# Kernel optimization log

Measured on AMD Instinct MI355X. Metric: run time of the kernel, lower is better.

Reference implementation:

```python
import jax, jax.numpy as jnp
import numpy as np

B, S, DQK, DV, H = 4, 2048, 128, 128, 8


def setup_inputs() -> dict:
    key = jax.random.key(0)
    ks = jax.random.split(key, 9)
    s = 0.02
    return {
        "query": jax.random.normal(ks[0], (B, S, DQK), jnp.float32),
        "key": jax.random.normal(ks[1], (B, S, DQK), jnp.float32),
        "value": jax.random.normal(ks[2], (B, S, DV), jnp.float32),
        "WQ": jax.random.normal(ks[3], (DQK, H * DQK), jnp.float32) * s,
        "bQ": jax.random.normal(ks[4], (H * DQK,), jnp.float32) * s,
        "WK": jax.random.normal(ks[5], (DQK, H * DQK), jnp.float32) * s,
        "bK": jax.random.normal(ks[6], (H * DQK,), jnp.float32) * s,
        "WV": jax.random.normal(ks[7], (DV, H * DV), jnp.float32) * s,
        "bV": jax.random.normal(ks[8], (H * DV,), jnp.float32) * s,
    }


def reference(query, key, value, WQ, bQ, WK, bK, WV, bV):
    b, qn, dqk = query.shape
    kn = key.shape[1]
    dv = value.shape[2]
    h = H
    # projections -> [b, n, h, d]
    Q = (query @ WQ + bQ).reshape(b, qn, h, dqk)
    K = (key @ WK + bK).reshape(b, kn, h, dqk)
    V = (value @ WV + bV).reshape(b, kn, h, dv)
    # abs(QK^T)/sqrt(dk) score -- non-standard, prevents flash kernels
    scores = jnp.abs(jnp.einsum("bqhd,bkhd->bhqk", Q, K)) / jnp.sqrt(
        jnp.asarray(dqk, query.dtype)
    )
    w = jax.nn.softmax(scores, axis=-1)  # [b,h,q,k]
    # (complex cast +0j in the original is numerically a no-op on real V)
    out = jnp.einsum("bhqk,bkhd->bqhd", w, V).reshape(b, qn, h * dv)
    return out
```

## Files before the change

### kernel.cpp

```cpp
#include <hip/hip_runtime.h>
#include <hip/hip_bf16.h>

#define B_ 4
#define S_ 2048
#define D_ 128
#define H_ 8

typedef __attribute__((ext_vector_type(8))) short bf16x8;
typedef __attribute__((ext_vector_type(4))) float f32x4;

__device__ __forceinline__ short f2bf(float f) {
  union { float f; unsigned u; } v; v.f = f;
  unsigned u = v.u;
  unsigned r = (u + 0x7FFFu + ((u >> 16) & 1u)) >> 16;
  return (short)r;
}

__device__ __forceinline__ short4 pack4(f32x4 p) {
  union { __hip_bfloat162 h2[2]; short4 s4; } u;
  u.h2[0] = __float22bfloat162_rn(make_float2(p[0], p[1]));
  u.h2[1] = __float22bfloat162_rn(make_float2(p[2], p[3]));
  return u.s4;
}

__global__ __launch_bounds__(256) void prep(
    const float* __restrict__ WQ, const float* __restrict__ WK, const float* __restrict__ WV,
    short* __restrict__ FQ, short* __restrict__ FK, short* __restrict__ FV) {
  __shared__ float tile[64][65];
  int bw = blockIdx.x >> 5;
  int tl = blockIdx.x & 31;
  int n0 = (tl & 15) * 64, k0 = (tl >> 4) * 64;
  const float* W = (bw == 0) ? WQ : (bw == 1) ? WK : WV;
  short* WF = (bw == 0) ? FQ : (bw == 1) ? FK : FV;
#pragma unroll
  for (int i = 0; i < 16; ++i) {
    int cix = threadIdx.x + 256 * i;
    int rr = cix >> 6, cc = cix & 63;
    tile[rr][cc] = W[(k0 + rr) * 1024 + n0 + cc];
  }
  __syncthreads();
#pragma unroll
  for (int i = 0; i < 16; ++i) {
    int cix = threadIdx.x + 256 * i;
    int rr = cix >> 6, cc = cix & 63;
    int n = n0 + rr, k = k0 + cc;
    size_t off = (size_t)(n >> 7) * 16384
               + (size_t)(((n >> 4) & 7) * 4 + (k >> 5)) * 512
               + ((k >> 3) & 3) * 128 + (n & 15) * 8 + (k & 7);
    WF[off] = f2bf(tile[cc][rr]);
  }
}

template <int MODE>
__device__ __forceinline__ void proj_tile(const float* __restrict__ X,
                                          const short* __restrict__ WF,
                                          const float* __restrict__ bias,
                                          short* __restrict__ out,
                                          int mtile, int ntile,
                                          short* sA) {
  int tid = threadIdx.x;
  int lane = tid & 63, w = tid >> 6;
  int l15 = lane & 15, l4 = lane >> 4;
  int m0 = mtile * 128, n0 = ntile * 128;

#pragma unroll
  for (int j = 0; j < 8; ++j) {
    int f = w * 8 + j;
    const float* src = X + (size_t)(m0 + (f >> 2) * 16 + l15) * 128 + (f & 3) * 32 + l4 * 8;
    float4 v0 = *(const float4*)src;
    float4 v1 = *(const float4*)(src + 4);
    union { struct { short4 lo, hi; } s; bf16x8 v; } u;
    u.s.lo = pack4((f32x4){v0.x, v0.y, v0.z, v0.w});
    u.s.hi = pack4((f32x4){v1.x, v1.y, v1.z, v1.w});
    *(bf16x8*)(sA + f * 512 + lane * 8) = u.v;
  }

  int wr = w >> 1, wc = w & 1;

  const short* wfb = WF + (size_t)ntile * 16384 + wc * 8192 + lane * 8;
  bf16x8 b[16];
#pragma unroll
  for (int q = 0; q < 16; ++q)
    b[q] = *(const bf16x8*)(wfb + q * 512);

  __syncthreads();

  f32x4 acc[4][4];
#pragma unroll
  for (int mi = 0; mi < 4; ++mi)
#pragma unroll
    for (int ni = 0; ni < 4; ++ni) acc[mi][ni] = (f32x4){0.f, 0.f, 0.f, 0.f};

#pragma unroll
  for (int mi = 0; mi < 4; ++mi) {
    bf16x8 a[4];
#pragma unroll
    for (int st = 0; st < 4; ++st)
      a[st] = *(const bf16x8*)(sA + ((wr * 4 + mi) * 4 + st) * 512 + lane * 8);
#pragma unroll
    for (int ni = 0; ni < 4; ++ni) {
#pragma unroll
      for (int st = 0; st < 4; ++st) {
        if (MODE <= 1)
          acc[mi][ni] = __builtin_amdgcn_mfma_f32_16x16x32_bf16(b[ni * 4 + st], a[st], acc[mi][ni], 0, 0, 0);
        else
          acc[mi][ni] = __builtin_amdgcn_mfma_f32_16x16x32_bf16(a[st], b[ni * 4 + st], acc[mi][ni], 0, 0, 0);
      }
    }
  }

  if (MODE == 0) {
#pragma unroll
    for (int mi = 0; mi < 4; ++mi) {
      int sg = m0 + wr * 64 + mi * 16 + l15;
      int bb = sg >> 11, s = sg & 2047;
      short* orow = out + ((size_t)(bb * H_ + ntile) * S_ + s) * D_;
#pragma unroll
      for (int ni = 0; ni < 4; ++ni) {
        int d0 = wc * 64 + ni * 16 + l4 * 4;
        float4 bv = *(const float4*)(bias + n0 + d0);
        f32x4 t = acc[mi][ni];
        t[0] += bv.x; t[1] += bv.y; t[2] += bv.z; t[3] += bv.w;
        *(short4*)(orow + d0) = pack4(t);
      }
    }
  } else if (MODE == 1) {
#pragma unroll
    for (int mi = 0; mi < 4; ++mi) {
      int key = m0 + wr * 64 + mi * 16 + l15;
      int bb = key >> 11, k = key & 2047;
      size_t base = (size_t)(bb * H_ + ntile) * (S_ * D_) + (size_t)(k >> 6) * 8192
                  + ((k >> 4) & 3) * 4 * 512 + (k & 15) * 8;
#pragma unroll
      for (int ni = 0; ni < 4; ++ni) {
        int d0 = wc * 64 + ni * 16 + l4 * 4;
        float4 bv = *(const float4*)(bias + n0 + d0);
        f32x4 t = acc[mi][ni];
        t[0] += bv.x; t[1] += bv.y; t[2] += bv.z; t[3] += bv.w;
        size_t off = base + (size_t)(d0 >> 5) * 512 + ((d0 >> 3) & 3) * 128 + (d0 & 7);
        *(short4*)(out + off) = pack4(t);
      }
    }
  } else {
#pragma unroll
    for (int ni = 0; ni < 4; ++ni) {
      int d = wc * 64 + ni * 16 + l15;
      float bvs = bias[n0 + d];
#pragma unroll
      for (int mi = 0; mi < 4; ++mi) {
        int sg0 = m0 + wr * 64 + mi * 16 + l4 * 4;
        int bb = sg0 >> 11, s0 = sg0 & 2047;
        f32x4 t = acc[mi][ni];
        t[0] += bvs; t[1] += bvs; t[2] += bvs; t[3] += bvs;
        size_t off = (size_t)(bb * H_ + ntile) * (S_ * D_)
                   + (size_t)(s0 >> 6) * 8192
                   + (size_t)((d >> 4) * 2 + ((s0 >> 5) & 1)) * 512
                   + ((s0 >> 3) & 3) * 128 + (d & 15) * 8
                   + (s0 & 7);
        *(short4*)(out + off) = pack4(t);
      }
    }
  }
}

__global__ __launch_bounds__(256, 3) void proj3(
    const float* __restrict__ xq, const float* __restrict__ xk, const float* __restrict__ xv,
    const short* __restrict__ wtq, const short* __restrict__ wtk, const short* __restrict__ wtv,
    const float* __restrict__ bQ, const float* __restrict__ bK, const float* __restrict__ bV,
    short* __restrict__ Qp, short* __restrict__ Kf, short* __restrict__ Vf) {
  __shared__ short sA[16384];
  int work = (blockIdx.x & 7) * 192 + (blockIdx.x >> 3);
  int which = work >> 9;
  int t = work & 511;
  int mtile = t >> 3, ntile = t & 7;
  if (which == 0)      proj_tile<0>(xq, wtq, bQ, Qp, mtile, ntile, sA);
  else if (which == 1) proj_tile<1>(xk, wtk, bK, Kf, mtile, ntile, sA);
  else                 proj_tile<2>(xv, wtv, bV, Vf, mtile, ntile, sA);
}

#define PSTR 72

#define HSTEP(KC, KN, H, DOISS)                                                \
  {                                                                            \
    if (DOISS) {                                                               \
      _Pragma("unroll") for (int j = 0; j < 8; ++j)                            \
        KN[j] = *(const bf16x8*)(kfb + ((H) + 1) * 4096 + j * 512);            \
    }                                                                          \
    bf16x8 bv[8];                                                              \
    _Pragma("unroll") for (int j = 0; j < 8; ++j)                              \
      bv[j] = *(const bf16x8*)(vfb + ((H) >> 1) * 8192 + (j * 2 + ((H) & 1)) * 512); \
    __builtin_amdgcn_sched_barrier(0);                                         \
    f32x4 s0[2], s1[2];                                                        \
    __builtin_amdgcn_s_setprio(1);                                             \
    _Pragma("unroll") for (int m = 0; m < 2; ++m) {                            \
      s0[m] = (f32x4){0.f, 0.f, 0.f, 0.f};                                     \
      s1[m] = (f32x4){0.f, 0.f, 0.f, 0.f};                                     \
      _Pragma("unroll") for (int st = 0; st < 4; ++st) {                       \
        s0[m] = __builtin_amdgcn_mfma_f32_16x16x32_bf16(KC[m * 4 + st], aq[0][st], s0[m], 0, 0, 0); \
        s1[m] = __builtin_amdgcn_mfma_f32_16x16x32_bf16(KC[m * 4 + st], aq[1][st], s1[m], 0, 0, 0); \
      }                                                                        \
    }                                                                          \
    __builtin_amdgcn_s_setprio(0);                                             \
    bf16x8 ap0, ap1;                                                           \
    _Pragma("unroll") for (int m = 0; m < 2; ++m) {                            \
      _Pragma("unroll") for (int r = 0; r < 4; ++r) {                          \
        float p = __builtin_amdgcn_exp2f(fabsf(s0[m][r]) * SC2);               \
        ls0 += p;                                                              \
        s0[m][r] = p;                                                          \
      }                                                                        \
      *(short4*)(pw + l15 * PSTR + m * 16 + l4 * 4) = pack4(s0[m]);            \
    }                                                                          \
    ap0 = *(const bf16x8*)(pw + l15 * PSTR + l4 * 8);                          \
    _Pragma("unroll") for (int m = 0; m < 2; ++m) {                            \
      _Pragma("unroll") for (int r = 0; r < 4; ++r) {                          \
        float p = __builtin_amdgcn_exp2f(fabsf(s1[m][r]) * SC2);               \
        ls1 += p;                                                              \
        s1[m][r] = p;                                                          \
      }                                                                        \
      *(short4*)(pw + l15 * PSTR + m * 16 + l4 * 4) = pack4(s1[m]);            \
    }                                                                          \
    ap1 = *(const bf16x8*)(pw + l15 * PSTR + l4 * 8);                          \
    __builtin_amdgcn_s_setprio(1);                                             \
    _Pragma("unroll") for (int t8 = 0; t8 < 8; ++t8) {                         \
      o0[t8] = __builtin_amdgcn_mfma_f32_16x16x32_bf16(ap0, bv[t8], o0[t8], 0, 0, 0); \
      o1[t8] = __builtin_amdgcn_mfma_f32_16x16x32_bf16(ap1, bv[t8], o1[t8], 0, 0, 0); \
    }                                                                          \
    __builtin_amdgcn_s_setprio(0);                                             \
  }

__global__ __launch_bounds__(256, 2) void attn(const short* __restrict__ Qp,
                                               const short* __restrict__ Kf,
                                               const short* __restrict__ Vf,
                                               float* __restrict__ out) {
  __shared__ short sP[4 * 16 * PSTR];

  int tid = threadIdx.x;
  int lane = tid & 63, w = tid >> 6;
  int xcd = blockIdx.x & 7;
  int idx = blockIdx.x >> 3;
  int bh  = xcd * 4 + (idx & 3);
  int qt  = idx >> 2;
  int q0 = qt * 128;
  int l15 = lane & 15, l4 = lane >> 4;

  const short* Qbase = Qp + (size_t)bh * S_ * D_;
  const short* kfb = Kf + (size_t)bh * S_ * D_ + lane * 8;
  const short* vfb = Vf + (size_t)bh * S_ * D_ + lane * 8;

  bf16x8 aq[2][4];
#pragma unroll
  for (int g = 0; g < 2; ++g)
#pragma unroll
    for (int st = 0; st < 4; ++st)
      aq[g][st] = *(const bf16x8*)(Qbase + (q0 + w * 32 + g * 16 + l15) * D_ + l4 * 8 + 32 * st);

  f32x4 o0[8], o1[8];
#pragma unroll
  for (int t = 0; t < 8; ++t) {
    o0[t] = (f32x4){0.f, 0.f, 0.f, 0.f};
    o1[t] = (f32x4){0.f, 0.f, 0.f, 0.f};
  }
  float ls0 = 0.f, ls1 = 0.f;

  const float SC2 = 0.127530637f;
  short* pw = sP + w * 16 * PSTR;

  bf16x8 kfA[8], kfB[8];
#pragma unroll
  for (int j = 0; j < 8; ++j)
    kfA[j] = *(const bf16x8*)(kfb + j * 512);

  for (int t = 0; t < 32; ++t) {
    HSTEP(kfA, kfB, 2 * t, true);
    HSTEP(kfB, kfA, 2 * t + 1, (t < 31));
  }

  ls0 += __shfl_xor(ls0, 16);
  ls0 += __shfl_xor(ls0, 32);
  ls1 += __shfl_xor(ls1, 16);
  ls1 += __shfl_xor(ls1, 32);
  float inv0[4], inv1[4];
#pragma unroll
  for (int r = 0; r < 4; ++r) {
    inv0[r] = 1.f / __shfl(ls0, l4 * 4 + r);
    inv1[r] = 1.f / __shfl(ls1, l4 * 4 + r);
  }

  int bb = bh >> 3, h = bh & 7;
#pragma unroll
  for (int t = 0; t < 8; ++t) {
#pragma unroll
    for (int r = 0; r < 4; ++r) {
      int qA = q0 + w * 32 + l4 * 4 + r;
      int qB = qA + 16;
      out[((size_t)(bb * S_ + qA)) * (H_ * D_) + h * D_ + t * 16 + l15] = o0[t][r] * inv0[r];
      out[((size_t)(bb * S_ + qB)) * (H_ * D_) + h * D_ + t * 16 + l15] = o1[t][r] * inv1[r];
    }
  }
}

extern "C" void kernel_launch(void* const* d_in, const int* in_sizes, int n_in,
                              void* d_out, int out_size, void* d_ws, size_t ws_size,
                              hipStream_t stream) {
  (void)in_sizes; (void)n_in; (void)out_size; (void)ws_size;
  const float* q  = (const float*)d_in[0];
  const float* k  = (const float*)d_in[1];
  const float* v  = (const float*)d_in[2];
  const float* WQ = (const float*)d_in[3];
  const float* bQ = (const float*)d_in[4];
  const float* WK = (const float*)d_in[5];
  const float* bK = (const float*)d_in[6];
  const float* WV = (const float*)d_in[7];
  const float* bV = (const float*)d_in[8];

  const int NW = D_ * H_ * D_;
  const int NP = B_ * H_ * S_ * D_;

  short* ws  = (short*)d_ws;
  short* wtq = ws;
  short* wtk = wtq + NW;
  short* wtv = wtk + NW;
  short* Qp  = wtv + NW;
  short* Kf  = Qp + NP;
  short* Vf  = Kf + NP;

  prep<<<96, 256, 0, stream>>>(WQ, WK, WV, wtq, wtk, wtv);

  proj3<<<1536, 256, 0, stream>>>(q, k, v, wtq, wtk, wtv, bQ, bK, bV, Qp, Kf, Vf);

  attn<<<512, 256, 0, stream>>>(Qp, Kf, Vf, (float*)d_out);
}
```

Measured before the change: 184.4 us.

## Stage K/V tiles in LDS via async global-to-LDS DMA with double buffering

The attention kernel now uses 512-thread blocks covering 256 queries. K and V tiles are shared through LDS and filled with global_load_lds DMA into double buffers, instead of each wave loading K/V from global memory into registers on its own. This cuts redundant global/L2 traffic for K/V, since 8 waves now reuse each tile. In exchange it adds a __syncthreads per iteration, more LDS use (about 82KB) and LDS read pressure, and halves the grid to 256 blocks, which may leave some CUs underfilled.

```diff
diff --git a/kernel.cpp b/kernel.cpp
--- a/kernel.cpp
+++ b/kernel.cpp
@@ -21,6 +21,12 @@
   u.h2[0] = __float22bfloat162_rn(make_float2(p[0], p[1]));
   u.h2[1] = __float22bfloat162_rn(make_float2(p[2], p[3]));
   return u.s4;
+}
+
+__device__ __forceinline__ void dma16(const short* g, short* l) {
+  __builtin_amdgcn_global_load_lds(
+      (const __attribute__((address_space(1))) unsigned int*)g,
+      (__attribute__((address_space(3))) unsigned int*)l, 16, 0, 0);
 }
 
 __global__ __launch_bounds__(256) void prep(
@@ -180,59 +186,49 @@
 
 #define PSTR 72
 
-#define HSTEP(KC, KN, H, DOISS)                                                \
-  {                                                                            \
-    if (DOISS) {                                                               \
-      _Pragma("unroll") for (int j = 0; j < 8; ++j)                            \
-        KN[j] = *(const bf16x8*)(kfb + ((H) + 1) * 4096 + j * 512);            \
+#define QK_H(KR)                                                               \
+  _Pragma("unroll") for (int m = 0; m < 2; ++m) {                              \
+    s0[m] = (f32x4){0.f, 0.f, 0.f, 0.f};                                       \
+    s1[m] = (f32x4){0.f, 0.f, 0.f, 0.f};                                       \
+    _Pragma("unroll") for (int st = 0; st < 4; ++st) {                         \
+      s0[m] = __builtin_amdgcn_mfma_f32_16x16x32_bf16(KR[m * 4 + st], aq[0][st], s0[m], 0, 0, 0); \
+      s1[m] = __builtin_amdgcn_mfma_f32_16x16x32_bf16(KR[m * 4 + st], aq[1][st], s1[m], 0, 0, 0); \
     }                                                                          \
-    bf16x8 bv[8];                                                              \
-    _Pragma("unroll") for (int j = 0; j < 8; ++j)                              \
-      bv[j] = *(const bf16x8*)(vfb + ((H) >> 1) * 8192 + (j * 2 + ((H) & 1)) * 512); \
-    __builtin_amdgcn_sched_barrier(0);                                         \
-    f32x4 s0[2], s1[2];                                                        \
-    __builtin_amdgcn_s_setprio(1);                                             \
-    _Pragma("unroll") for (int m = 0; m < 2; ++m) {                            \
-      s0[m] = (f32x4){0.f, 0.f, 0.f, 0.f};                                     \
-      s1[m] = (f32x4){0.f, 0.f, 0.f, 0.f};                                     \
-      _Pragma("unroll") for (int st = 0; st < 4; ++st) {                       \
-        s0[m] = __builtin_amdgcn_mfma_f32_16x16x32_bf16(KC[m * 4 + st], aq[0][st], s0[m], 0, 0, 0); \
-        s1[m] = __builtin_amdgcn_mfma_f32_16x16x32_bf16(KC[m * 4 + st], aq[1][st], s1[m], 0, 0, 0); \
-      }                                                                        \
+  }
+
+#define SM_H()                                                                 \
+  _Pragma("unroll") for (int m = 0; m < 2; ++m) {                              \
+    _Pragma("unroll") for (int r = 0; r < 4; ++r) {                            \
+      float p = __builtin_amdgcn_exp2f(fabsf(s0[m][r]) * SC2);                 \
+      ls0 += p;                                                                \
+      s0[m][r] = p;                                                            \
     }                                                                          \
-    __builtin_amdgcn_s_setprio(0);                                             \
-    bf16x8 ap0, ap1;                                                           \
-    _Pragma("unroll") for (int m = 0; m < 2; ++m) {                            \
-      _Pragma("unroll") for (int r = 0; r < 4; ++r) {                          \
-        float p = __builtin_amdgcn_exp2f(fabsf(s0[m][r]) * SC2);               \
-        ls0 += p;                                                              \
-        s0[m][r] = p;                                                          \
-      }                                                                        \
-      *(short4*)(pw + l15 * PSTR + m * 16 + l4 * 4) = pack4(s0[m]);            \
+    *(short4*)(pw + l15 * PSTR + m * 16 + l4 * 4) = pack4(s0[m]);              \
+  }                                                                            \
+  ap0 = *(const bf16x8*)(pw + l15 * PSTR + l4 * 8);                            \
+  _Pragma("unroll") for (int m = 0; m < 2; ++m) {                              \
+    _Pragma("unroll") for (int r = 0; r < 4; ++r) {                            \
+      float p = __builtin_amdgcn_exp2f(fabsf(s1[m][r]) * SC2);                 \
+      ls1 += p;                                                                \
+      s1[m][r] = p;                                                            \
     }                                                                          \
-    ap0 = *(const bf16x8*)(pw + l15 * PSTR + l4 * 8);                          \
-    _Pragma("unroll") for (int m = 0; m < 2; ++m) {                            \
-      _Pragma("unroll") for (int r = 0; r < 4; ++r) {                          \
-        float p = __builtin_amdgcn_exp2f(fabsf(s1[m][r]) * SC2);               \
-        ls1 += p;                                                              \
-        s1[m][r] = p;                                                          \
-      }                                                                        \
-      *(short4*)(pw + l15 * PSTR + m * 16 + l4 * 4) = pack4(s1[m]);            \
-    }                                                                          \
-    ap1 = *(const bf16x8*)(pw + l15 * PSTR + l4 * 8);                          \
-    __builtin_amdgcn_s_setprio(1);                                             \
-    _Pragma("unroll") for (int t8 = 0; t8 < 8; ++t8) {                         \
-      o0[t8] = __builtin_amdgcn_mfma_f32_16x16x32_bf16(ap0, bv[t8], o0[t8], 0, 0, 0); \
-      o1[t8] = __builtin_amdgcn_mfma_f32_16x16x32_bf16(ap1, bv[t8], o1[t8], 0, 0, 0); \
-    }                                                                          \
-    __builtin_amdgcn_s_setprio(0);                                             \
-  }
-
-__global__ __launch_bounds__(256, 2) void attn(const short* __restrict__ Qp,
+    *(short4*)(pw + l15 * PSTR + m * 16 + l4 * 4) = pack4(s1[m]);              \
+  }                                                                            \
+  ap1 = *(const bf16x8*)(pw + l15 * PSTR + l4 * 8);
+
+#define PV_H()                                                                 \
+  _Pragma("unroll") for (int t8 = 0; t8 < 8; ++t8) {                           \
+    o0[t8] = __builtin_amdgcn_mfma_f32_16x16x32_bf16(ap0, bv[t8], o0[t8], 0, 0, 0); \
+    o1[t8] = __builtin_amdgcn_mfma_f32_16x16x32_bf16(ap1, bv[t8], o1[t8], 0, 0, 0); \
+  }
+
+__global__ __launch_bounds__(512, 2) void attn(const short* __restrict__ Qp,
                                                const short* __restrict__ Kf,
                                                const short* __restrict__ Vf,
                                                float* __restrict__ out) {
-  __shared__ short sP[4 * 16 * PSTR];
+  __shared__ short sK0[8192], sK1[8192];
+  __shared__ short sV0[8192], sV1[8192];
+  __shared__ short sP[8 * 16 * PSTR];
 
   int tid = threadIdx.x;
   int lane = tid & 63, w = tid >> 6;
@@ -240,12 +236,17 @@
   int idx = blockIdx.x >> 3;
   int bh  = xcd * 4 + (idx & 3);
   int qt  = idx >> 2;
-  int q0 = qt * 128;
+  int q0  = qt * 256;
   int l15 = lane & 15, l4 = lane >> 4;
 
   const short* Qbase = Qp + (size_t)bh * S_ * D_;
-  const short* kfb = Kf + (size_t)bh * S_ * D_ + lane * 8;
-  const short* vfb = Vf + (size_t)bh * S_ * D_ + lane * 8;
+  const short* kgs = Kf + (size_t)bh * S_ * D_ + 2 * w * 512 + lane * 8;
+  const short* vgs = Vf + (size_t)bh * S_ * D_ + 2 * w * 512 + lane * 8;
+
+  dma16(kgs,       sK0 + 2 * w * 512);
+  dma16(kgs + 512, sK0 + (2 * w + 1) * 512);
+  dma16(vgs,       sV0 + 2 * w * 512);
+  dma16(vgs + 512, sV0 + (2 * w + 1) * 512);
 
   bf16x8 aq[2][4];
 #pragma unroll
@@ -265,14 +266,53 @@
   const float SC2 = 0.127530637f;
   short* pw = sP + w * 16 * PSTR;
 
-  bf16x8 kfA[8], kfB[8];
-#pragma unroll
-  for (int j = 0; j < 8; ++j)
-    kfA[j] = *(const bf16x8*)(kfb + j * 512);
+  __syncthreads();
 
   for (int t = 0; t < 32; ++t) {
-    HSTEP(kfA, kfB, 2 * t, true);
-    HSTEP(kfB, kfA, 2 * t + 1, (t < 31));
+    const short* sKc = (t & 1) ? sK1 : sK0;
+    const short* sVc = (t & 1) ? sV1 : sV0;
+    if (t < 31) {
+      short* sKn = (t & 1) ? sK0 : sK1;
+      short* sVn = (t & 1) ? sV0 : sV1;
+      const short* kn = kgs + (size_t)(t + 1) * 8192;
+      const short* vn = vgs + (size_t)(t + 1) * 8192;
+      dma16(kn,       sKn + 2 * w * 512);
+      dma16(kn + 512, sKn + (2 * w + 1) * 512);
+      dma16(vn,       sVn + 2 * w * 512);
+      dma16(vn + 512, sVn + (2 * w + 1) * 512);
+    }
+    bf16x8 kA[8], kB[8], bv[8];
+#pragma unroll
+    for (int j = 0; j < 8; ++j)
+      kA[j] = *(const bf16x8*)(sKc + j * 512 + lane * 8);
+#pragma unroll
+    for (int j = 0; j < 8; ++j)
+      kB[j] = *(const bf16x8*)(sKc + 4096 + j * 512 + lane * 8);
+#pragma unroll
+    for (int j = 0; j < 8; ++j)
+      bv[j] = *(const bf16x8*)(sVc + (2 * j) * 512 + lane * 8);
+    __builtin_amdgcn_sched_barrier(0);
+
+    f32x4 s0[2], s1[2];
+    bf16x8 ap0, ap1;
+    __builtin_amdgcn_s_setprio(1);
+    QK_H(kA);
+    __builtin_amdgcn_s_setprio(0);
+    SM_H();
+    __builtin_amdgcn_s_setprio(1);
+    PV_H();
+    __builtin_amdgcn_s_setprio(0);
+#pragma unroll
+    for (int j = 0; j < 8; ++j)
+      bv[j] = *(const bf16x8*)(sVc + (2 * j + 1) * 512 + lane * 8);
+    __builtin_amdgcn_s_setprio(1);
+    QK_H(kB);
+    __builtin_amdgcn_s_setprio(0);
+    SM_H();
+    __builtin_amdgcn_s_setprio(1);
+    PV_H();
+    __builtin_amdgcn_s_setprio(0);
+    __syncthreads();
   }
 
   ls0 += __shfl_xor(ls0, 16);
@@ -328,5 +368,5 @@
 
   proj3<<<1536, 256, 0, stream>>>(q, k, v, wtq, wtk, wtv, bQ, bK, bV, Qp, Kf, Vf);
 
-  attn<<<512, 256, 0, stream>>>(Qp, Kf, Vf, (float*)d_out);
-}
+  attn<<<256, 512, 0, stream>>>(Qp, Kf, Vf, (float*)d_out);
+}
```

Result: no change. 184.0 us (-0.3%).
